# Kernel optimization log

Hardware: AMD Instinct MI355X
Metric: run time of the kernel (lower is better)

The kernel has to match this reference:

```python
import jax, jax.numpy as jnp
import numpy as np

I, H, O, T = 64, 512, 1, 65536


def setup_inputs() -> dict:
    key = jax.random.key(0)
    ks = jax.random.split(key, 12)
    s = 1.0 / np.sqrt(H)
    u = lambda k, shape: jax.random.uniform(k, shape, jnp.float32, -s, s)
    return {
        "input_seq": jax.random.normal(ks[0], (T, I), jnp.float32),
        "W_ih1": u(ks[1], (4 * H, I)), "W_hh1": u(ks[2], (4 * H, H)),
        "b_ih1": u(ks[3], (4 * H,)), "b_hh1": u(ks[4], (4 * H,)),
        "W_ih2": u(ks[5], (4 * H, H)), "W_hh2": u(ks[6], (4 * H, H)),
        "b_ih2": u(ks[7], (4 * H,)), "b_hh2": u(ks[8], (4 * H,)),
        "W_out": u(ks[9], (O, H)), "b_out": u(ks[10], (O,)),
    }


def _lstm_cell(x, h, c, W_ih, W_hh, b_ih, b_hh):
    # torch.nn.LSTMCell gate order: input, forget, cell(g), output
    gates = x @ W_ih.T + b_ih + h @ W_hh.T + b_hh  # [4H]
    i, f, g, o = jnp.split(gates, 4)
    c_new = jax.nn.sigmoid(f) * c + jax.nn.sigmoid(i) * jnp.tanh(g)
    h_new = jax.nn.sigmoid(o) * jnp.tanh(c_new)
    return h_new, c_new


def reference(input_seq, W_ih1, W_hh1, b_ih1, b_hh1,
              W_ih2, W_hh2, b_ih2, b_hh2, W_out, b_out):
    h = input_seq.dtype
    zeros = jnp.zeros((H,), h)

    def step(carry, x_t):
        h1, c1, h2, c2 = carry
        h1, c1 = _lstm_cell(x_t, h1, c1, W_ih1, W_hh1, b_ih1, b_hh1)
        h2, c2 = _lstm_cell(h1, h2, c2, W_ih2, W_hh2, b_ih2, b_hh2)
        return (h1, c1, h2, c2), None

    (h1, c1, h2, c2), _ = jax.lax.scan(step, (zeros, zeros, zeros, zeros), input_seq)
    # final output = linear(last h2), as in the original forward
    return h2 @ W_out.T + b_out
```

## Files before the change

kernel.cpp:

```cpp
#include <hip/hip_runtime.h>

#define IDIM  64
#define HDIM  512
#define T_LEN 65536
#define NWG   128
#define NTHR  512

__device__ unsigned long long g_h1[2][HDIM];
__device__ unsigned long long g_h2[2][HDIM];

__device__ __forceinline__ unsigned long long pack(float v, int k) {
  return ((unsigned long long)(unsigned)k << 32) | (unsigned long long)__float_as_uint(v);
}

__global__ void lstm_init() {
  int t = threadIdx.x;
  for (int e = t; e < HDIM; e += blockDim.x) {
    g_h1[0][e] = 0xFFFFFFFF00000000ull;
    g_h1[1][e] = 0xFFFFFFFF00000000ull;
    g_h2[0][e] = 0xFFFFFFFF00000000ull;
    g_h2[1][e] = 0x0000000000000000ull;
  }
}

__global__ __launch_bounds__(NTHR)
__attribute__((amdgpu_waves_per_eu(2, 2)))
void lstm_main(
    const float* __restrict__ x_seq,
    const float* __restrict__ W_ih1, const float* __restrict__ W_hh1,
    const float* __restrict__ b_ih1, const float* __restrict__ b_hh1,
    const float* __restrict__ W_ih2, const float* __restrict__ W_hh2,
    const float* __restrict__ b_ih2, const float* __restrict__ b_hh2,
    const float* __restrict__ W_out, const float* __restrict__ b_out,
    float* __restrict__ out)
{
  const int wg   = blockIdx.x;
  const int tid  = threadIdx.x;
  const int wave = tid >> 6;
  const int role = wave >> 2;
  const int lane = tid & 63;
  const int g    = lane >> 4;
  const int s    = lane & 15;
  const int j    = wg * 4 + (wave & 3);
  const int r    = g * HDIM + j;

  float w[64];
  if (role == 0) {
#pragma unroll
    for (int m = 0; m < 36; ++m) {
      int e = s * 36 + m;
      w[m] = (e < HDIM) ? W_hh1[(size_t)r * HDIM + e]
                        : W_ih1[(size_t)r * IDIM + (e - HDIM)];
    }
#pragma unroll
    for (int m = 0; m < 36; ++m) asm volatile("" : "+v"(w[m]));
  } else {
#pragma unroll
    for (int c = 0; c < 16; ++c) {
#pragma unroll
      for (int i = 0; i < 4; ++i) {
        int er = s * 64 + ((c + s) & 15) * 4 + i;
        w[c * 4 + i] = (er < HDIM) ? W_ih2[(size_t)r * HDIM + er]
                                   : W_hh2[(size_t)r * HDIM + (er - HDIM)];
      }
    }
#pragma unroll
    for (int m = 0; m < 64; ++m) asm volatile("" : "+v"(w[m]));
  }
  const float bsel = (role == 0) ? (b_ih1[r] + b_hh1[r]) : (b_ih2[r] + b_hh2[r]);

  float cst = 0.f;
  int bud = 1 << 24;

  __shared__ __align__(16) float vec[2][HDIM + IDIM + HDIM];

  for (int k = 0; k <= T_LEN; ++k) {
    const unsigned expect = (unsigned)(k - 1);
    const int p1  = (k + 1) & 1;
    const int p2  = k & 1;
    const int buf = k & 1;

    float xv = 0.f;
    if (tid < IDIM && k < T_LEN) xv = x_seq[(size_t)k * IDIM + tid];

    unsigned long long a = 0, b = 0;
    bool ok1 = false, ok2 = false;
    do {
      if (!ok1) {
        a = __hip_atomic_load(&g_h1[p1][tid], __ATOMIC_RELAXED, __HIP_MEMORY_SCOPE_AGENT);
        ok1 = ((unsigned)(a >> 32) == expect);
      }
      if (!ok2) {
        b = __hip_atomic_load(&g_h2[p2][tid], __ATOMIC_RELAXED, __HIP_MEMORY_SCOPE_AGENT);
        ok2 = ((unsigned)(b >> 32) == expect);
      }
    } while ((!ok1 || !ok2) && --bud > 0);

    vec[buf][tid] = __uint_as_float((unsigned)a);
    vec[buf][HDIM + IDIM + tid] = __uint_as_float((unsigned)b);
    if (tid < IDIM) vec[buf][HDIM + tid] = xv;
    __syncthreads();

    const bool active = (role == 0) ? (k < T_LEN) : (k > 0);
    if (active) {
      float acc = 0.f;
      if (role == 0) {
#pragma unroll
        for (int mc = 0; mc < 9; ++mc) {
          const float4 hv = *reinterpret_cast<const float4*>(&vec[buf][s * 36 + mc * 4]);
          acc = fmaf(w[mc * 4 + 0], hv.x, acc);
          acc = fmaf(w[mc * 4 + 1], hv.y, acc);
          acc = fmaf(w[mc * 4 + 2], hv.z, acc);
          acc = fmaf(w[mc * 4 + 3], hv.w, acc);
        }
      } else {
        const int vb = (s < 8) ? 0 : IDIM;
#pragma unroll
        for (int c = 0; c < 16; ++c) {
          const int off = s * 64 + ((c + s) & 15) * 4 + vb;
          const float4 hv = *reinterpret_cast<const float4*>(&vec[buf][off]);
          acc = fmaf(w[c * 4 + 0], hv.x, acc);
          acc = fmaf(w[c * 4 + 1], hv.y, acc);
          acc = fmaf(w[c * 4 + 2], hv.z, acc);
          acc = fmaf(w[c * 4 + 3], hv.w, acc);
        }
      }
      acc += __shfl_xor(acc, 8, 16);
      acc += __shfl_xor(acc, 4, 16);
      acc += __shfl_xor(acc, 2, 16);
      acc += __shfl_xor(acc, 1, 16);

      const float xs  = acc + bsel;
      const float xin = (g == 2) ? 2.f * xs : xs;
      const float sgm = 1.f / (1.f + expf(-xin));
      const float act = (g == 2) ? 2.f * sgm - 1.f : sgm;
      const float ai = __shfl(act, 0, 64);
      const float af = __shfl(act, 16, 64);
      const float ag = __shfl(act, 32, 64);
      const float ao = __shfl(act, 48, 64);
      cst = af * cst + ai * ag;
      const float tc = 2.f / (1.f + expf(-2.f * cst)) - 1.f;
      const float hv = ao * tc;
      if (lane == 0) {
        if (role == 0)
          __hip_atomic_store(&g_h1[k & 1][j], pack(hv, k),
                             __ATOMIC_RELAXED, __HIP_MEMORY_SCOPE_AGENT);
        else
          __hip_atomic_store(&g_h2[(k + 1) & 1][j], pack(hv, k),
                             __ATOMIC_RELAXED, __HIP_MEMORY_SCOPE_AGENT);
      }
    }
  }

  if (wg == 0 && wave == 0) {
    float acc = 0.f;
    int bud2 = 1 << 24;
#pragma unroll
    for (int e = 0; e < HDIM / 64; ++e) {
      const int idx = lane + e * 64;
      unsigned long long u;
      do {
        u = __hip_atomic_load(&g_h2[1][idx], __ATOMIC_RELAXED, __HIP_MEMORY_SCOPE_AGENT);
      } while ((unsigned)(u >> 32) != (unsigned)T_LEN && --bud2 > 0);
      acc = fmaf(W_out[idx], __uint_as_float((unsigned)u), acc);
    }
    acc += __shfl_xor(acc, 32, 64);
    acc += __shfl_xor(acc, 16, 64);
    acc += __shfl_xor(acc, 8, 64);
    acc += __shfl_xor(acc, 4, 64);
    acc += __shfl_xor(acc, 2, 64);
    acc += __shfl_xor(acc, 1, 64);
    if (lane == 0) out[0] = acc + b_out[0];
  }
}

extern "C" void kernel_launch(void* const* d_in, const int* in_sizes, int n_in,
                              void* d_out, int out_size, void* d_ws, size_t ws_size,
                              hipStream_t stream) {
  const float* x_seq = (const float*)d_in[0];
  const float* W_ih1 = (const float*)d_in[1];
  const float* W_hh1 = (const float*)d_in[2];
  const float* b_ih1 = (const float*)d_in[3];
  const float* b_hh1 = (const float*)d_in[4];
  const float* W_ih2 = (const float*)d_in[5];
  const float* W_hh2 = (const float*)d_in[6];
  const float* b_ih2 = (const float*)d_in[7];
  const float* b_hh2 = (const float*)d_in[8];
  const float* W_out = (const float*)d_in[9];
  const float* b_out = (const float*)d_in[10];
  float* out = (float*)d_out;

  hipLaunchKernelGGL(lstm_init, dim3(1), dim3(256), 0, stream);
  hipLaunchKernelGGL(lstm_main, dim3(NWG), dim3(NTHR), 0, stream,
                     x_seq, W_ih1, W_hh1, b_ih1, b_hh1,
                     W_ih2, W_hh2, b_ih2, b_hh2, W_out, b_out, out);
}
```

Baseline: 129.3 ms.

## Pack per-workgroup h1/h2 outputs into tagged 16-byte chunks for cross-WG exchange

Replaces the per-element 64-bit tagged atomics for h1 and h2 with per-workgroup 16-byte chunks, each holding a step tag and three floats. They are written by three threads after an extra block barrier and polled with dwordx4 loads that bypass the caches via sc0 sc1. The aim is to cut the number of polled global locations and store transactions per step, from 1024 per-element words to 384 chunks. In exchange it adds a second __syncthreads per step and relies on 16-byte stores being seen atomically, with the tag and data in the same chunk.

```diff
diff --git a/kernel.cpp b/kernel.cpp
--- a/kernel.cpp
+++ b/kernel.cpp
@@ -5,21 +5,35 @@
 #define T_LEN 65536
 #define NWG   128
 #define NTHR  512
-
-__device__ unsigned long long g_h1[2][HDIM];
-__device__ unsigned long long g_h2[2][HDIM];
-
-__device__ __forceinline__ unsigned long long pack(float v, int k) {
-  return ((unsigned long long)(unsigned)k << 32) | (unsigned long long)__float_as_uint(v);
+#define NCHUNK (NWG * 3)
+
+typedef unsigned int u32x4 __attribute__((ext_vector_type(4)));
+
+__device__ u32x4 g_post[2][NWG][8];
+
+__device__ __forceinline__ u32x4 load_chunk(const u32x4* p) {
+  u32x4 r;
+  unsigned long long a = (unsigned long long)p;
+  asm volatile("global_load_dwordx4 %0, %1, off sc0 sc1\n\t"
+               "s_waitcnt vmcnt(0)"
+               : "=v"(r) : "v"(a) : "memory");
+  return r;
+}
+__device__ __forceinline__ void store_chunk(u32x4* p, u32x4 v) {
+  unsigned long long a = (unsigned long long)p;
+  asm volatile("global_store_dwordx4 %0, %1, off sc0 sc1"
+               :: "v"(a), "v"(v) : "memory");
 }
 
 __global__ void lstm_init() {
   int t = threadIdx.x;
-  for (int e = t; e < HDIM; e += blockDim.x) {
-    g_h1[0][e] = 0xFFFFFFFF00000000ull;
-    g_h1[1][e] = 0xFFFFFFFF00000000ull;
-    g_h2[0][e] = 0xFFFFFFFF00000000ull;
-    g_h2[1][e] = 0x0000000000000000ull;
+  for (int w = t; w < NWG; w += blockDim.x) {
+    for (int i = 0; i < 3; ++i) {
+      u32x4 m1 = {0xFFFFFFFFu, 0u, 0u, 0u};
+      u32x4 nv = {0xFFFFFFFEu, 0u, 0u, 0u};
+      g_post[1][w][i] = m1;
+      g_post[0][w][i] = nv;
+    }
   }
 }
 
@@ -73,56 +87,57 @@
   int bud = 1 << 24;
 
   __shared__ __align__(16) float vec[2][HDIM + IDIM + HDIM];
+  __shared__ float hbuf[8];
+
+  const int cw = tid / 3;
+  const int ci = tid - cw * 3;
 
   for (int k = 0; k <= T_LEN; ++k) {
     const unsigned expect = (unsigned)(k - 1);
-    const int p1  = (k + 1) & 1;
-    const int p2  = k & 1;
+    const int pb  = (k + 1) & 1;
     const int buf = k & 1;
 
-    float xv = 0.f;
-    if (tid < IDIM && k < T_LEN) xv = x_seq[(size_t)k * IDIM + tid];
-
-    unsigned long long a = 0, b = 0;
-    bool ok1 = false, ok2 = false;
-    do {
-      if (!ok1) {
-        a = __hip_atomic_load(&g_h1[p1][tid], __ATOMIC_RELAXED, __HIP_MEMORY_SCOPE_AGENT);
-        ok1 = ((unsigned)(a >> 32) == expect);
-      }
-      if (!ok2) {
-        b = __hip_atomic_load(&g_h2[p2][tid], __ATOMIC_RELAXED, __HIP_MEMORY_SCOPE_AGENT);
-        ok2 = ((unsigned)(b >> 32) == expect);
-      }
-    } while ((!ok1 || !ok2) && --bud > 0);
-
-    vec[buf][tid] = __uint_as_float((unsigned)a);
-    vec[buf][HDIM + IDIM + tid] = __uint_as_float((unsigned)b);
-    if (tid < IDIM) vec[buf][HDIM + tid] = xv;
+    if (tid < NCHUNK) {
+      const u32x4* src = &g_post[pb][cw][ci];
+      u32x4 ch = load_chunk(src);
+      while (ch[0] != expect && --bud > 0) ch = load_chunk(src);
+      const float f0 = __uint_as_float(ch[1]);
+      const float f1 = __uint_as_float(ch[2]);
+      const float f2 = __uint_as_float(ch[3]);
+      const int b1 = cw * 4;
+      const int b2 = HDIM + IDIM + cw * 4;
+      if (ci == 0)      { vec[buf][b1+0] = f0; vec[buf][b1+1] = f1; vec[buf][b1+2] = f2; }
+      else if (ci == 1) { vec[buf][b1+3] = f0; vec[buf][b2+0] = f1; vec[buf][b2+1] = f2; }
+      else              { vec[buf][b2+2] = f0; vec[buf][b2+3] = f1; }
+    } else if (tid < NCHUNK + IDIM) {
+      if (k < T_LEN)
+        vec[buf][HDIM + (tid - NCHUNK)] = x_seq[(size_t)k * IDIM + (tid - NCHUNK)];
+    }
     __syncthreads();
 
+    float hv = 0.f;
     const bool active = (role == 0) ? (k < T_LEN) : (k > 0);
     if (active) {
       float acc = 0.f;
       if (role == 0) {
 #pragma unroll
         for (int mc = 0; mc < 9; ++mc) {
-          const float4 hv = *reinterpret_cast<const float4*>(&vec[buf][s * 36 + mc * 4]);
-          acc = fmaf(w[mc * 4 + 0], hv.x, acc);
-          acc = fmaf(w[mc * 4 + 1], hv.y, acc);
-          acc = fmaf(w[mc * 4 + 2], hv.z, acc);
-          acc = fmaf(w[mc * 4 + 3], hv.w, acc);
+          const float4 hvv = *reinterpret_cast<const float4*>(&vec[buf][s * 36 + mc * 4]);
+          acc = fmaf(w[mc * 4 + 0], hvv.x, acc);
+          acc = fmaf(w[mc * 4 + 1], hvv.y, acc);
+          acc = fmaf(w[mc * 4 + 2], hvv.z, acc);
+          acc = fmaf(w[mc * 4 + 3], hvv.w, acc);
         }
       } else {
         const int vb = (s < 8) ? 0 : IDIM;
 #pragma unroll
         for (int c = 0; c < 16; ++c) {
           const int off = s * 64 + ((c + s) & 15) * 4 + vb;
-          const float4 hv = *reinterpret_cast<const float4*>(&vec[buf][off]);
-          acc = fmaf(w[c * 4 + 0], hv.x, acc);
-          acc = fmaf(w[c * 4 + 1], hv.y, acc);
-          acc = fmaf(w[c * 4 + 2], hv.z, acc);
-          acc = fmaf(w[c * 4 + 3], hv.w, acc);
+          const float4 hvv = *reinterpret_cast<const float4*>(&vec[buf][off]);
+          acc = fmaf(w[c * 4 + 0], hvv.x, acc);
+          acc = fmaf(w[c * 4 + 1], hvv.y, acc);
+          acc = fmaf(w[c * 4 + 2], hvv.z, acc);
+          acc = fmaf(w[c * 4 + 3], hvv.w, acc);
         }
       }
       acc += __shfl_xor(acc, 8, 16);
@@ -140,15 +155,22 @@
       const float ao = __shfl(act, 48, 64);
       cst = af * cst + ai * ag;
       const float tc = 2.f / (1.f + expf(-2.f * cst)) - 1.f;
-      const float hv = ao * tc;
-      if (lane == 0) {
-        if (role == 0)
-          __hip_atomic_store(&g_h1[k & 1][j], pack(hv, k),
-                             __ATOMIC_RELAXED, __HIP_MEMORY_SCOPE_AGENT);
-        else
-          __hip_atomic_store(&g_h2[(k + 1) & 1][j], pack(hv, k),
-                             __ATOMIC_RELAXED, __HIP_MEMORY_SCOPE_AGENT);
+      hv = ao * tc;
+    }
+    if (lane == 0) hbuf[wave] = hv;
+    __syncthreads();
+
+    if (tid < 3) {
+      const unsigned tag = (unsigned)k;
+      u32x4 o;
+      if (tid == 0) {
+        o[0]=tag; o[1]=__float_as_uint(hbuf[0]); o[2]=__float_as_uint(hbuf[1]); o[3]=__float_as_uint(hbuf[2]);
+      } else if (tid == 1) {
+        o[0]=tag; o[1]=__float_as_uint(hbuf[3]); o[2]=__float_as_uint(hbuf[4]); o[3]=__float_as_uint(hbuf[5]);
+      } else {
+        o[0]=tag; o[1]=__float_as_uint(hbuf[6]); o[2]=__float_as_uint(hbuf[7]); o[3]=0u;
       }
+      store_chunk(&g_post[buf][wg][tid], o);
     }
   }
 
@@ -156,13 +178,18 @@
     float acc = 0.f;
     int bud2 = 1 << 24;
 #pragma unroll
-    for (int e = 0; e < HDIM / 64; ++e) {
-      const int idx = lane + e * 64;
-      unsigned long long u;
-      do {
-        u = __hip_atomic_load(&g_h2[1][idx], __ATOMIC_RELAXED, __HIP_MEMORY_SCOPE_AGENT);
-      } while ((unsigned)(u >> 32) != (unsigned)T_LEN && --bud2 > 0);
-      acc = fmaf(W_out[idx], __uint_as_float((unsigned)u), acc);
+    for (int rep = 0; rep < 2; ++rep) {
+      const int w2 = lane + rep * 64;
+      const u32x4* p1 = &g_post[0][w2][1];
+      const u32x4* p2 = &g_post[0][w2][2];
+      u32x4 c1 = load_chunk(p1);
+      while (c1[0] != (unsigned)T_LEN && --bud2 > 0) c1 = load_chunk(p1);
+      u32x4 c2 = load_chunk(p2);
+      while (c2[0] != (unsigned)T_LEN && --bud2 > 0) c2 = load_chunk(p2);
+      acc = fmaf(W_out[4 * w2 + 0], __uint_as_float(c1[2]), acc);
+      acc = fmaf(W_out[4 * w2 + 1], __uint_as_float(c1[3]), acc);
+      acc = fmaf(W_out[4 * w2 + 2], __uint_as_float(c2[1]), acc);
+      acc = fmaf(W_out[4 * w2 + 3], __uint_as_float(c2[2]), acc);
     }
     acc += __shfl_xor(acc, 32, 64);
     acc += __shfl_xor(acc, 16, 64);
```

After: 155.2 ms. +20.0%, slower.

## Broadcast hidden states into per-workgroup mailboxes to avoid shared polling

Applied to the files above, without the earlier changes.

Replaces the single global h1/h2 exchange arrays with a per-workgroup mailbox array. Each producing wave now has all 64 lanes write its tagged hidden value into the mailboxes of all 128 workgroups. Every workgroup then spins only on its own private copy, which is meant to cut contention and coherence traffic from 128 workgroups polling the same cache lines each step. The cost is a large rise in store traffic: every hidden element is written 128 times per timestep, which could eat into the latency-bound step time.

```diff
diff --git a/kernel.cpp b/kernel.cpp
--- a/kernel.cpp
+++ b/kernel.cpp
@@ -5,22 +5,23 @@
 #define T_LEN 65536
 #define NWG   128
 #define NTHR  512
-
-__device__ unsigned long long g_h1[2][HDIM];
-__device__ unsigned long long g_h2[2][HDIM];
+#define NSLOT (2 * HDIM)
+
+__device__ unsigned long long g_mb[2][NWG][NSLOT];
 
 __device__ __forceinline__ unsigned long long pack(float v, int k) {
   return ((unsigned long long)(unsigned)k << 32) | (unsigned long long)__float_as_uint(v);
 }
 
 __global__ void lstm_init() {
-  int t = threadIdx.x;
-  for (int e = t; e < HDIM; e += blockDim.x) {
-    g_h1[0][e] = 0xFFFFFFFF00000000ull;
-    g_h1[1][e] = 0xFFFFFFFF00000000ull;
-    g_h2[0][e] = 0xFFFFFFFF00000000ull;
-    g_h2[1][e] = 0x0000000000000000ull;
-  }
+  const int t = threadIdx.x;
+  for (int w = 0; w < NWG; ++w)
+    for (int e = t; e < HDIM; e += blockDim.x) {
+      g_mb[1][w][e]        = 0xFFFFFFFF00000000ull;
+      g_mb[0][w][e]        = 0xFFFFFFFE00000000ull;
+      g_mb[0][w][HDIM + e] = 0xFFFFFFFF00000000ull;
+      g_mb[1][w][HDIM + e] = 0x0000000000000000ull;
+    }
 }
 
 __global__ __launch_bounds__(NTHR)
@@ -83,15 +84,17 @@
     float xv = 0.f;
     if (tid < IDIM && k < T_LEN) xv = x_seq[(size_t)k * IDIM + tid];
 
+    unsigned long long* s1 = &g_mb[p1][wg][tid];
+    unsigned long long* s2 = &g_mb[p2][wg][HDIM + tid];
     unsigned long long a = 0, b = 0;
     bool ok1 = false, ok2 = false;
     do {
       if (!ok1) {
-        a = __hip_atomic_load(&g_h1[p1][tid], __ATOMIC_RELAXED, __HIP_MEMORY_SCOPE_AGENT);
+        a = __hip_atomic_load(s1, __ATOMIC_RELAXED, __HIP_MEMORY_SCOPE_AGENT);
         ok1 = ((unsigned)(a >> 32) == expect);
       }
       if (!ok2) {
-        b = __hip_atomic_load(&g_h2[p2][tid], __ATOMIC_RELAXED, __HIP_MEMORY_SCOPE_AGENT);
+        b = __hip_atomic_load(s2, __ATOMIC_RELAXED, __HIP_MEMORY_SCOPE_AGENT);
         ok2 = ((unsigned)(b >> 32) == expect);
       }
     } while ((!ok1 || !ok2) && --bud > 0);
@@ -141,14 +144,14 @@
       cst = af * cst + ai * ag;
       const float tc = 2.f / (1.f + expf(-2.f * cst)) - 1.f;
       const float hv = ao * tc;
-      if (lane == 0) {
-        if (role == 0)
-          __hip_atomic_store(&g_h1[k & 1][j], pack(hv, k),
-                             __ATOMIC_RELAXED, __HIP_MEMORY_SCOPE_AGENT);
-        else
-          __hip_atomic_store(&g_h2[(k + 1) & 1][j], pack(hv, k),
-                             __ATOMIC_RELAXED, __HIP_MEMORY_SCOPE_AGENT);
-      }
+
+      const int vidx = (role == 0) ? j : (HDIM + j);
+      const int par  = (role == 0) ? (k & 1) : ((k + 1) & 1);
+      const unsigned long long rec = pack(hv, k);
+      __hip_atomic_store(&g_mb[par][lane][vidx], rec,
+                         __ATOMIC_RELAXED, __HIP_MEMORY_SCOPE_AGENT);
+      __hip_atomic_store(&g_mb[par][lane + 64][vidx], rec,
+                         __ATOMIC_RELAXED, __HIP_MEMORY_SCOPE_AGENT);
     }
   }
 
@@ -160,7 +163,7 @@
       const int idx = lane + e * 64;
       unsigned long long u;
       do {
-        u = __hip_atomic_load(&g_h2[1][idx], __ATOMIC_RELAXED, __HIP_MEMORY_SCOPE_AGENT);
+        u = __hip_atomic_load(&g_mb[1][0][HDIM + idx], __ATOMIC_RELAXED, __HIP_MEMORY_SCOPE_AGENT);
       } while ((unsigned)(u >> 32) != (unsigned)T_LEN && --bud2 > 0);
       acc = fmaf(W_out[idx], __uint_as_float((unsigned)u), acc);
     }
```

Result: slower. 398.9 ms (+208.4%).

## Halve workgroup count by computing two hidden units per wave

Applied to the files above, without the earlier changes.

Each wave now holds weights for two hidden units (j0, j1) and computes both gate dot products, activations and cell updates, so the grid drops from 128 to 64 workgroups. The aim is to cut the number of participants in the per-step global spin-wait handshake and to interleave two independent FMA chains for ILP. In exchange, weight register usage doubles (up to 128 floats per lane) under a 2-waves-per-EU bound, which risks spills, and the per-step arithmetic on each CU doubles.

```diff
diff --git a/kernel.cpp b/kernel.cpp
--- a/kernel.cpp
+++ b/kernel.cpp
@@ -3,7 +3,7 @@
 #define IDIM  64
 #define HDIM  512
 #define T_LEN 65536
-#define NWG   128
+#define NWG   64
 #define NTHR  512
 
 __device__ unsigned long long g_h1[2][HDIM];
@@ -41,35 +41,38 @@
   const int lane = tid & 63;
   const int g    = lane >> 4;
   const int s    = lane & 15;
-  const int j    = wg * 4 + (wave & 3);
-  const int r    = g * HDIM + j;
-
-  float w[64];
+  const int j0   = wg * 8 + (wave & 3) * 2;
+  const int j1   = j0 + 1;
+  const int rA   = g * HDIM + j0;
+  const int rB   = g * HDIM + j1;
+
+  float wA[64], wB[64];
   if (role == 0) {
 #pragma unroll
     for (int m = 0; m < 36; ++m) {
       int e = s * 36 + m;
-      w[m] = (e < HDIM) ? W_hh1[(size_t)r * HDIM + e]
-                        : W_ih1[(size_t)r * IDIM + (e - HDIM)];
-    }
-#pragma unroll
-    for (int m = 0; m < 36; ++m) asm volatile("" : "+v"(w[m]));
+      wA[m] = (e < HDIM) ? W_hh1[(size_t)rA * HDIM + e] : W_ih1[(size_t)rA * IDIM + (e - HDIM)];
+      wB[m] = (e < HDIM) ? W_hh1[(size_t)rB * HDIM + e] : W_ih1[(size_t)rB * IDIM + (e - HDIM)];
+    }
+#pragma unroll
+    for (int m = 0; m < 36; ++m) { asm volatile("" : "+v"(wA[m])); asm volatile("" : "+v"(wB[m])); }
   } else {
 #pragma unroll
     for (int c = 0; c < 16; ++c) {
 #pragma unroll
       for (int i = 0; i < 4; ++i) {
         int er = s * 64 + ((c + s) & 15) * 4 + i;
-        w[c * 4 + i] = (er < HDIM) ? W_ih2[(size_t)r * HDIM + er]
-                                   : W_hh2[(size_t)r * HDIM + (er - HDIM)];
-      }
-    }
-#pragma unroll
-    for (int m = 0; m < 64; ++m) asm volatile("" : "+v"(w[m]));
-  }
-  const float bsel = (role == 0) ? (b_ih1[r] + b_hh1[r]) : (b_ih2[r] + b_hh2[r]);
-
-  float cst = 0.f;
+        wA[c*4+i] = (er < HDIM) ? W_ih2[(size_t)rA * HDIM + er] : W_hh2[(size_t)rA * HDIM + (er - HDIM)];
+        wB[c*4+i] = (er < HDIM) ? W_ih2[(size_t)rB * HDIM + er] : W_hh2[(size_t)rB * HDIM + (er - HDIM)];
+      }
+    }
+#pragma unroll
+    for (int m = 0; m < 64; ++m) { asm volatile("" : "+v"(wA[m])); asm volatile("" : "+v"(wB[m])); }
+  }
+  const float bselA = (role == 0) ? (b_ih1[rA] + b_hh1[rA]) : (b_ih2[rA] + b_hh2[rA]);
+  const float bselB = (role == 0) ? (b_ih1[rB] + b_hh1[rB]) : (b_ih2[rB] + b_hh2[rB]);
+
+  float cstA = 0.f, cstB = 0.f;
   int bud = 1 << 24;
 
   __shared__ __align__(16) float vec[2][HDIM + IDIM + HDIM];
@@ -103,15 +106,15 @@
 
     const bool active = (role == 0) ? (k < T_LEN) : (k > 0);
     if (active) {
-      float acc = 0.f;
+      float accA = 0.f, accB = 0.f;
       if (role == 0) {
 #pragma unroll
         for (int mc = 0; mc < 9; ++mc) {
           const float4 hv = *reinterpret_cast<const float4*>(&vec[buf][s * 36 + mc * 4]);
-          acc = fmaf(w[mc * 4 + 0], hv.x, acc);
-          acc = fmaf(w[mc * 4 + 1], hv.y, acc);
-          acc = fmaf(w[mc * 4 + 2], hv.z, acc);
-          acc = fmaf(w[mc * 4 + 3], hv.w, acc);
+          accA = fmaf(wA[mc*4+0], hv.x, accA); accB = fmaf(wB[mc*4+0], hv.x, accB);
+          accA = fmaf(wA[mc*4+1], hv.y, accA); accB = fmaf(wB[mc*4+1], hv.y, accB);
+          accA = fmaf(wA[mc*4+2], hv.z, accA); accB = fmaf(wB[mc*4+2], hv.z, accB);
+          accA = fmaf(wA[mc*4+3], hv.w, accA); accB = fmaf(wB[mc*4+3], hv.w, accB);
         }
       } else {
         const int vb = (s < 8) ? 0 : IDIM;
@@ -119,35 +122,43 @@
         for (int c = 0; c < 16; ++c) {
           const int off = s * 64 + ((c + s) & 15) * 4 + vb;
           const float4 hv = *reinterpret_cast<const float4*>(&vec[buf][off]);
-          acc = fmaf(w[c * 4 + 0], hv.x, acc);
-          acc = fmaf(w[c * 4 + 1], hv.y, acc);
-          acc = fmaf(w[c * 4 + 2], hv.z, acc);
-          acc = fmaf(w[c * 4 + 3], hv.w, acc);
+          accA = fmaf(wA[c*4+0], hv.x, accA); accB = fmaf(wB[c*4+0], hv.x, accB);
+          accA = fmaf(wA[c*4+1], hv.y, accA); accB = fmaf(wB[c*4+1], hv.y, accB);
+          accA = fmaf(wA[c*4+2], hv.z, accA); accB = fmaf(wB[c*4+2], hv.z, accB);
+          accA = fmaf(wA[c*4+3], hv.w, accA); accB = fmaf(wB[c*4+3], hv.w, accB);
         }
       }
-      acc += __shfl_xor(acc, 8, 16);
-      acc += __shfl_xor(acc, 4, 16);
-      acc += __shfl_xor(acc, 2, 16);
-      acc += __shfl_xor(acc, 1, 16);
-
-      const float xs  = acc + bsel;
-      const float xin = (g == 2) ? 2.f * xs : xs;
-      const float sgm = 1.f / (1.f + expf(-xin));
-      const float act = (g == 2) ? 2.f * sgm - 1.f : sgm;
-      const float ai = __shfl(act, 0, 64);
-      const float af = __shfl(act, 16, 64);
-      const float ag = __shfl(act, 32, 64);
-      const float ao = __shfl(act, 48, 64);
-      cst = af * cst + ai * ag;
-      const float tc = 2.f / (1.f + expf(-2.f * cst)) - 1.f;
-      const float hv = ao * tc;
+      accA += __shfl_xor(accA, 8, 16);  accB += __shfl_xor(accB, 8, 16);
+      accA += __shfl_xor(accA, 4, 16);  accB += __shfl_xor(accB, 4, 16);
+      accA += __shfl_xor(accA, 2, 16);  accB += __shfl_xor(accB, 2, 16);
+      accA += __shfl_xor(accA, 1, 16);  accB += __shfl_xor(accB, 1, 16);
+
+      const float xsA  = accA + bselA;
+      const float xsB  = accB + bselB;
+      const float xinA = (g == 2) ? 2.f * xsA : xsA;
+      const float xinB = (g == 2) ? 2.f * xsB : xsB;
+      const float sgmA = 1.f / (1.f + expf(-xinA));
+      const float sgmB = 1.f / (1.f + expf(-xinB));
+      const float actA = (g == 2) ? 2.f * sgmA - 1.f : sgmA;
+      const float actB = (g == 2) ? 2.f * sgmB - 1.f : sgmB;
+      const float aiA = __shfl(actA, 0, 64),  aiB = __shfl(actB, 0, 64);
+      const float afA = __shfl(actA, 16, 64), afB = __shfl(actB, 16, 64);
+      const float agA = __shfl(actA, 32, 64), agB = __shfl(actB, 32, 64);
+      const float aoA = __shfl(actA, 48, 64), aoB = __shfl(actB, 48, 64);
+      cstA = afA * cstA + aiA * agA;
+      cstB = afB * cstB + aiB * agB;
+      const float tcA = 2.f / (1.f + expf(-2.f * cstA)) - 1.f;
+      const float tcB = 2.f / (1.f + expf(-2.f * cstB)) - 1.f;
+      const float hvA = aoA * tcA;
+      const float hvB = aoB * tcB;
       if (lane == 0) {
-        if (role == 0)
-          __hip_atomic_store(&g_h1[k & 1][j], pack(hv, k),
-                             __ATOMIC_RELAXED, __HIP_MEMORY_SCOPE_AGENT);
-        else
-          __hip_atomic_store(&g_h2[(k + 1) & 1][j], pack(hv, k),
-                             __ATOMIC_RELAXED, __HIP_MEMORY_SCOPE_AGENT);
+        if (role == 0) {
+          __hip_atomic_store(&g_h1[k & 1][j0], pack(hvA, k), __ATOMIC_RELAXED, __HIP_MEMORY_SCOPE_AGENT);
+          __hip_atomic_store(&g_h1[k & 1][j1], pack(hvB, k), __ATOMIC_RELAXED, __HIP_MEMORY_SCOPE_AGENT);
+        } else {
+          __hip_atomic_store(&g_h2[(k + 1) & 1][j0], pack(hvA, k), __ATOMIC_RELAXED, __HIP_MEMORY_SCOPE_AGENT);
+          __hip_atomic_store(&g_h2[(k + 1) & 1][j1], pack(hvB, k), __ATOMIC_RELAXED, __HIP_MEMORY_SCOPE_AGENT);
+        }
       }
     }
   }
```

Result: slower. 151.2 ms (+16.9%).
